# Optimization experiments

Measured on AMD Instinct MI355X. Metric: run time of the kernel, lower is better.

The kernel has to match this reference:

```python
import jax, jax.numpy as jnp
import numpy as np

N = 100_000      # nodes
E = 3_200_000    # directed edges (avg degree 32)
F_IN = 503
C = 32           # GATConv out_channels, heads=1
NEG_SLOPE = 0.2  # PyG GATConv default


def setup_inputs() -> dict:
    key = jax.random.key(0)
    ks = jax.random.split(key, 14)
    x = jax.random.normal(ks[0], (N, F_IN), jnp.float32)
    edge_index = jax.random.randint(ks[1], (2, E), 0, N)
    edge_weight = jax.random.uniform(ks[2], (E, 1), jnp.float32)
    input_mask = jnp.ones((N, 1), jnp.float32)
    # GATConv params (heads=1)
    W_src = jax.random.normal(ks[3], (C, F_IN), jnp.float32) * 0.02
    att_src = jax.random.normal(ks[4], (C,), jnp.float32) * 0.1
    att_dst = jax.random.normal(ks[5], (C,), jnp.float32) * 0.1
    att_edge = jax.random.normal(ks[6], (C,), jnp.float32) * 0.1
    W_edge = jax.random.normal(ks[7], (C, 1), jnp.float32) * 0.1
    bias_conv = jnp.zeros((C,), jnp.float32)
    # dense heads
    Wb = jax.random.normal(ks[8], (1, C), jnp.float32) * 0.1
    bb = jnp.zeros((1,), jnp.float32)
    Ww = jax.random.normal(ks[9], (1, C), jnp.float32) * 0.1
    bw = jnp.zeros((1,), jnp.float32)
    return {"x": x, "edge_index": edge_index, "edge_weight": edge_weight,
            "input_mask": input_mask, "W_src": W_src, "att_src": att_src,
            "att_dst": att_dst, "att_edge": att_edge, "W_edge": W_edge,
            "bias_conv": bias_conv, "Wb": Wb, "bb": bb, "Ww": Ww, "bw": bw}


def reference(x, edge_index, edge_weight, input_mask, W_src, att_src, att_dst,
              att_edge, W_edge, bias_conv, Wb, bb, Ww, bw):
    n = x.shape[0]
    xl = x @ W_src.T                       # [N, C] transformed node features
    a_src = xl @ att_src                   # [N] per-node source attention logit
    a_dst = xl @ att_dst                   # [N]
    src, dst = edge_index[0], edge_index[1]
    # add_self_loops=True with fill_value='mean' for edge_attr (PyG default)
    loop = jnp.arange(n)
    mean_attr = jnp.mean(edge_weight, axis=0, keepdims=True)      # [1,1]
    ea = jnp.concatenate([edge_weight, jnp.broadcast_to(mean_attr, (n, 1))], 0)
    s = jnp.concatenate([src, loop])       # [E+N]
    d = jnp.concatenate([dst, loop])
    a_edge = (ea @ W_edge.T) @ att_edge    # [E+N]
    alpha = jax.nn.leaky_relu(a_src[s] + a_dst[d] + a_edge, NEG_SLOPE)
    # softmax over incoming edges of each destination node
    amax = jax.ops.segment_max(alpha, d, num_segments=n)
    ex = jnp.exp(alpha - amax[d])
    denom = jax.ops.segment_sum(ex, d, num_segments=n)
    w = ex / denom[d]                      # [E+N] attention coeffs
    msg = xl[s] * w[:, None]               # [E+N, C]
    out = jax.ops.segment_sum(msg, d, num_segments=n) + bias_conv  # [N, C]
    h = jax.nn.relu(out)
    biases = (h @ Wb.T + bb) * input_mask  # [N, 1]
    weights = ((h[src] + h[dst]) * 0.5) @ Ww.T + bw  # [E, 1]
    return weights, biases
```

## Files before the change

kernel.cpp:

```cpp
#include <hip/hip_runtime.h>
#include <stdint.h>

#define NN 100000
#define NE 3200000
#define FIN 503
#define COUT 32
#define NSLOPE 0.2f

#define BSH 6
#define NB 1563
#define NGB 1563
#define NHB 400
#define EPB (NE / NHB)
#define NSB 7
#define MAXBE 2560

typedef __bf16 bf16x8 __attribute__((ext_vector_type(8)));
typedef float  f32x4  __attribute__((ext_vector_type(4)));

__device__ __forceinline__ unsigned short bf1(float f) {
    unsigned u = __float_as_uint(f);
    u = (u + 0x7FFFu + ((u >> 16) & 1u)) >> 16;
    return (unsigned short)u;
}
__device__ __forceinline__ float unbf(unsigned short h) {
    return __uint_as_float(((unsigned)h) << 16);
}

#define GR 64

__global__ __launch_bounds__(256)
void k_fused1(const float* __restrict__ x, const float* __restrict__ W,
              const float* __restrict__ att_s, const float* __restrict__ att_d,
              unsigned short* __restrict__ xlb,
              float* __restrict__ a_src, float* __restrict__ a_dst,
              const int* __restrict__ ei_dst, const float* __restrict__ ew,
              float* __restrict__ partial, unsigned* __restrict__ part,
              unsigned* __restrict__ done)
{
    __shared__ __align__(16) unsigned short xs[2][GR][40];
    __shared__ __align__(16) unsigned short ws[2][32][40];
    const int t = threadIdx.x;

    if (blockIdx.x >= NGB) {
        unsigned* h = (unsigned*)&xs[0][0][0];
        __shared__ float wsum[4];
        const int hb = blockIdx.x - NGB;
        for (int i = t; i < NB; i += 256) h[i] = 0u;
        __syncthreads();
        const int base = hb * EPB;
        for (int i = t; i < EPB; i += 256)
            atomicAdd(&h[ei_dst[base + i] >> BSH], 1u);
        const float4* ew4 = (const float4*)ew;
        float s = 0.f;
        for (int i = hb * 256 + t; i < NE / 4; i += NHB * 256) {
            float4 v = ew4[i];
            s += v.x + v.y + v.z + v.w;
        }
        #pragma unroll
        for (int off = 32; off > 0; off >>= 1) s += __shfl_xor(s, off);
        if ((t & 63) == 0) wsum[t >> 6] = s;
        __syncthreads();
        if (t == 0) partial[hb] = wsum[0] + wsum[1] + wsum[2] + wsum[3];
        for (int i = t; i < NB; i += 256)
            part[(size_t)hb * NB + i] = h[i];
        return;
    }

    if (blockIdx.x == 0 && t == 0) *done = 0u;
    unsigned short* os = &xs[0][0][0];
    const int wv = t >> 6, lane = t & 63;
    const int m16 = lane & 15, quad = lane >> 4;
    const int row0 = blockIdx.x * GR;
    const int srow = t >> 5;
    const int scol = t & 31;
    const int rowf = wv * 16 + m16;
    const int wrow = t >> 3;
    const int wc   = (t & 7) * 4;

    auto stageX = [&](int ch, int buf) {
        const int k = ch * 32 + scol;
        const bool ok = (k < FIN);
        #pragma unroll
        for (int p = 0; p < 8; ++p) {
            int r = p * 8 + srow;
            int rg = row0 + r;
            rg = (rg < NN) ? rg : (NN - 1);
            xs[buf][r][scol] = bf1(ok ? x[(size_t)rg * FIN + k] : 0.f);
        }
    };
    auto stageW = [&](int ch, int buf) {
        const int kb = ch * 32 + wc;
        #pragma unroll
        for (int j = 0; j < 4; ++j) {
            int k = kb + j;
            ws[buf][wrow][wc + j] = bf1((k < FIN) ? W[(size_t)wrow * FIN + k] : 0.f);
        }
    };

    f32x4 acc0 = {0.f, 0.f, 0.f, 0.f};
    f32x4 acc1 = {0.f, 0.f, 0.f, 0.f};

    stageX(0, 0);
    stageW(0, 0);
    for (int ch = 0; ch < 16; ++ch) {
        __syncthreads();
        if (ch < 15) {
            stageX(ch + 1, (ch + 1) & 1);
            stageW(ch + 1, (ch + 1) & 1);
        }
        bf16x8 af  = *(const bf16x8*)&xs[ch & 1][rowf][quad * 8];
        bf16x8 b0f = *(const bf16x8*)&ws[ch & 1][m16][quad * 8];
        bf16x8 b1f = *(const bf16x8*)&ws[ch & 1][m16 + 16][quad * 8];
        acc0 = __builtin_amdgcn_mfma_f32_16x16x32_bf16(af, b0f, acc0, 0, 0, 0);
        acc1 = __builtin_amdgcn_mfma_f32_16x16x32_bf16(af, b1f, acc1, 0, 0, 0);
    }

    #pragma unroll
    for (int r = 0; r < 4; ++r) {
        int rr = wv * 16 + quad * 4 + r;
        os[rr * 40 + m16]      = bf1(acc0[r]);
        os[rr * 40 + 16 + m16] = bf1(acc1[r]);
    }
    __syncthreads();
    {
        int r = t >> 2, c0 = (t & 3) * 8;
        int grow = row0 + r;
        uint4 o = *(const uint4*)&os[r * 40 + c0];
        float s = 0.f, dd = 0.f;
        const unsigned short* oh = (const unsigned short*)&o;
        #pragma unroll
        for (int j = 0; j < 8; ++j) {
            float v = unbf(oh[j]);
            s  += v * att_s[c0 + j];
            dd += v * att_d[c0 + j];
        }
        s  += __shfl_xor(s, 1, 4);  s  += __shfl_xor(s, 2, 4);
        dd += __shfl_xor(dd, 1, 4); dd += __shfl_xor(dd, 2, 4);
        if (grow < NN) {
            *(uint4*)&xlb[(size_t)grow * COUT + c0] = o;
            if ((t & 3) == 0) { a_src[grow] = s; a_dst[grow] = dd; }
        }
    }
}

__global__ __launch_bounds__(256)
void k_scan(unsigned* __restrict__ part, unsigned* __restrict__ colsum,
            unsigned* __restrict__ done, const float* __restrict__ partial,
            const float* __restrict__ W_edge, const float* __restrict__ att_e,
            float* __restrict__ stats, unsigned* __restrict__ bbase)
{
    const int t = threadIdx.x;
    const int bkt = blockIdx.x * 256 + t;
    if (bkt < NB) {
        unsigned run = 0u;
        #pragma unroll 1
        for (int s = 0; s < NHB; s += 8) {
            unsigned v[8];
            #pragma unroll
            for (int j = 0; j < 8; ++j) v[j] = part[(size_t)(s + j) * NB + bkt];
            #pragma unroll
            for (int j = 0; j < 8; ++j) {
                part[(size_t)(s + j) * NB + bkt] = run;
                run += v[j];
            }
        }
        colsum[bkt] = run;
    }
    __threadfence();
    __syncthreads();
    __shared__ unsigned winner;
    if (t == 0) winner = atomicAdd(done, 1u);
    __syncthreads();
    if (winner != NSB - 1) return;

    __shared__ float fs[256];
    fs[t] = (t < NHB ? partial[t] : 0.f) + (t + 256 < NHB ? partial[t + 256] : 0.f);
    __syncthreads();
    for (int off = 128; off > 0; off >>= 1) {
        if (t < off) fs[t] += fs[t + off];
        __syncthreads();
    }
    if (t == 0) {
        stats[0] = fs[0];
        float k = 0.f;
        for (int c = 0; c < COUT; ++c) k += W_edge[c] * att_e[c];
        stats[1] = k;
    }
    __syncthreads();
    __shared__ unsigned sm[256];
    __shared__ unsigned carry;
    if (t == 0) carry = 0u;
    __syncthreads();
    for (int c0 = 0; c0 < NB; c0 += 256) {
        int i = c0 + t;
        unsigned cv = (i < NB) ? atomicAdd(&colsum[i], 0u) : 0u;
        sm[t] = cv;
        for (int off = 1; off < 256; off <<= 1) {
            __syncthreads();
            unsigned tv = (t >= off) ? sm[t - off] : 0u;
            __syncthreads();
            sm[t] += tv;
        }
        __syncthreads();
        if (i < NB) bbase[i] = carry + sm[t] - cv;
        __syncthreads();
        if (t == 0) carry += sm[255];
        __syncthreads();
    }
    if (t == 0) bbase[NB] = carry;
}

__global__ __launch_bounds__(256)
void k_scatter(const int* __restrict__ ei, const float* __restrict__ ew,
               const float* __restrict__ a_src, const float* __restrict__ stats,
               const unsigned* __restrict__ part, const unsigned* __restrict__ bbase,
               uint2* __restrict__ csr)
{
    __shared__ unsigned cur[NB];
    const int b = blockIdx.x;
    const int t = threadIdx.x;
    for (int i = t; i < NB; i += 256)
        cur[i] = bbase[i] + part[(size_t)b * NB + i];
    __syncthreads();
    const float kc = stats[1];
    const int base = b * EPB;
    for (int i = t; i < EPB; i += 256) {
        int e = base + i;
        int s = ei[e];
        int d = ei[NE + e];
        float pre = a_src[s] + kc * ew[e];
        unsigned pos = atomicAdd(&cur[d >> BSH], 1u);
        csr[pos] = make_uint2((unsigned)s | ((unsigned)(d & 63) << 20),
                              __float_as_uint(pre));
    }
}

__global__ __launch_bounds__(256)
void k_aggr(const uint2* __restrict__ csr, const unsigned* __restrict__ bbase,
            const float* __restrict__ a_src, const float* __restrict__ a_dst,
            const unsigned short* __restrict__ xlb, const float* __restrict__ stats,
            const float* __restrict__ bias_conv, const float* __restrict__ Wb,
            const float* __restrict__ bb, const float* __restrict__ Ww,
            const float* __restrict__ mask, float* __restrict__ out_b,
            float* __restrict__ hw)
{
    __shared__ uint2 rec[MAXBE];
    __shared__ unsigned seg[65], cur[64];
    const int t = threadIdx.x;
    const int b = blockIdx.x;
    const int jb = (int)bbase[b];
    int ne = (int)bbase[b + 1] - jb;
    if (ne > MAXBE) ne = MAXBE;

    if (t < 64) cur[t] = 0u;
    __syncthreads();
    for (int i = t; i < ne; i += 256)
        atomicAdd(&cur[csr[jb + i].x >> 20], 1u);
    __syncthreads();
    if (t < 64) {
        unsigned v = cur[t];
        unsigned s = v;
        #pragma unroll
        for (int off = 1; off < 64; off <<= 1) {
            unsigned u = __shfl_up(s, off, 64);
            if (t >= off) s += u;
        }
        seg[t + 1] = s;
        cur[t] = s - v;
        if (t == 0) seg[0] = 0u;
    }
    __syncthreads();
    for (int i = t; i < ne; i += 256) {
        uint2 r = csr[jb + i];
        unsigned pos = atomicAdd(&cur[r.x >> 20], 1u);
        rec[pos] = r;
    }
    __syncthreads();

    const float kmean = stats[1] * (stats[0] * (1.f / NE));
    const int lane = t & 31;
    for (int dl = t >> 5; dl < 64; dl += 8) {
        int d = (b << BSH) + dl;
        if (d >= NN) continue;
        const float adv = a_dst[d];
        float a0 = a_src[d] + adv + kmean;
        a0 = (a0 > 0.f) ? a0 : NSLOPE * a0;
        const float ps = __expf(a0);
        float l = 0.f;
        float acc = ps * unbf(xlb[(size_t)d * COUT + lane]);
        const int j0 = (int)seg[dl], j1 = (int)seg[dl + 1];
        for (int tb = j0; tb < j1; tb += 32) {
            int j = tb + lane;
            float p = 0.f;
            if (j < j1) {
                uint2 en = rec[j];
                float a = __uint_as_float(en.y) + adv;
                a = (a > 0.f) ? a : NSLOPE * a;
                p = __expf(a);
                rec[j].y = __float_as_uint(p);
            }
            l += p;
            int cnte = min(32, j1 - tb);
            #pragma unroll 4
            for (int k = 0; k < cnte; ++k) {
                uint2 en = rec[tb + k];
                acc += __uint_as_float(en.y) *
                       unbf(xlb[(size_t)(en.x & 0xFFFFFu) * COUT + lane]);
            }
        }
        #pragma unroll
        for (int off = 16; off > 0; off >>= 1) l += __shfl_xor(l, off, 32);
        l += ps;
        float h = fmaxf(acc / l + bias_conv[lane], 0.f);
        float pb = h * Wb[lane];
        float pw = h * Ww[lane];
        #pragma unroll
        for (int off = 16; off > 0; off >>= 1) {
            pb += __shfl_xor(pb, off, 32);
            pw += __shfl_xor(pw, off, 32);
        }
        if (lane == 0) {
            out_b[d] = (pb + bb[0]) * mask[d];
            hw[d] = pw;
        }
    }
}

__global__ void k_weights(const int* __restrict__ ei, const float* __restrict__ hw,
                          const float* __restrict__ bw, float* __restrict__ out_w)
{
    int e4 = blockIdx.x * 256 + threadIdx.x;
    if (e4 < NE / 4) {
        int4 s4 = ((const int4*)ei)[e4];
        int4 d4 = ((const int4*)(ei + NE))[e4];
        float bwv = bw[0];
        float4 o;
        o.x = 0.5f * (hw[s4.x] + hw[d4.x]) + bwv;
        o.y = 0.5f * (hw[s4.y] + hw[d4.y]) + bwv;
        o.z = 0.5f * (hw[s4.z] + hw[d4.z]) + bwv;
        o.w = 0.5f * (hw[s4.w] + hw[d4.w]) + bwv;
        ((float4*)out_w)[e4] = o;
    }
}

extern "C" void kernel_launch(void* const* d_in, const int* in_sizes, int n_in,
                              void* d_out, int out_size, void* d_ws, size_t ws_size,
                              hipStream_t stream)
{
    const float* x        = (const float*)d_in[0];
    const int*   ei       = (const int*)d_in[1];
    const float* ew       = (const float*)d_in[2];
    const float* mask     = (const float*)d_in[3];
    const float* W_src    = (const float*)d_in[4];
    const float* att_src  = (const float*)d_in[5];
    const float* att_dst  = (const float*)d_in[6];
    const float* att_edge = (const float*)d_in[7];
    const float* W_edge   = (const float*)d_in[8];
    const float* bias_c   = (const float*)d_in[9];
    const float* Wb       = (const float*)d_in[10];
    const float* bb       = (const float*)d_in[11];
    const float* Ww       = (const float*)d_in[12];
    const float* bw       = (const float*)d_in[13];
    (void)in_sizes; (void)n_in; (void)out_size; (void)ws_size;

    char* wsp = (char*)d_ws;
    size_t off = 0;
    auto alloc = [&](size_t bytes) -> void* {
        void* p = wsp + off;
        off = (off + bytes + 255) & ~(size_t)255;
        return p;
    };
    unsigned short* xlb    = (unsigned short*)alloc((size_t)NN * COUT * 2);
    float*    a_src  = (float*)alloc((size_t)NN * 4);
    float*    a_dst  = (float*)alloc((size_t)NN * 4);
    float*    stats  = (float*)alloc(256);
    float*    partial= (float*)alloc((size_t)NHB * 4);
    unsigned* part   = (unsigned*)alloc((size_t)NHB * NB * 4);
    unsigned* colsum = (unsigned*)alloc((size_t)NB * 4);
    unsigned* bbase  = (unsigned*)alloc((size_t)(NB + 1) * 4);
    unsigned* done   = (unsigned*)alloc(256);
    uint2*    csr    = (uint2*)alloc((size_t)NE * 8);
    float*    hw     = (float*)alloc((size_t)NN * 4);

    float* out_w = (float*)d_out;
    float* out_b = out_w + NE;

    k_fused1  <<<NGB + NHB, 256, 0, stream>>>(x, W_src, att_src, att_dst,
                                              xlb, a_src, a_dst,
                                              ei + NE, ew, partial, part, done);
    k_scan    <<<NSB, 256, 0, stream>>>(part, colsum, done, partial, W_edge,
                                        att_edge, stats, bbase);
    k_scatter <<<NHB, 256, 0, stream>>>(ei, ew, a_src, stats, part, bbase, csr);
    k_aggr    <<<NB, 256, 0, stream>>>(csr, bbase, a_src, a_dst, xlb, stats,
                                       bias_c, Wb, bb, Ww, mask, out_b, hw);
    k_weights <<<NE / 4 / 256, 256, 0, stream>>>(ei, hw, bw, out_w);
}
```

Before: 546.2 us.

## Prefetch GEMM chunks into registers, widen histogram grid, split edge loop across half-waves

The GEMM staging now loads the next K-chunk into registers before the MFMAs and writes it to LDS afterwards, leaving one barrier per iteration, so global-load latency overlaps with compute. The histogram phase uses 1000 blocks instead of 400, and the final partial reduction loops over all partials. The aggregation kernel assigns one 64-lane wave per destination node, with each 32-lane half processing alternate edge batches and the halves combined by a cross-half shuffle. Costs are more registers in the GEMM and fewer destination nodes processed concurrently per block.

Result: slower. 611.3 us (+11.9%).

```diff
diff --git a/kernel.cpp b/kernel.cpp
--- a/kernel.cpp
+++ b/kernel.cpp
@@ -10,7 +10,7 @@
 #define BSH 6
 #define NB 1563
 #define NGB 1563
-#define NHB 400
+#define NHB 1000
 #define EPB (NE / NHB)
 #define NSB 7
 #define MAXBE 2560
@@ -78,42 +78,46 @@
     const int wrow = t >> 3;
     const int wc   = (t & 7) * 4;
 
-    auto stageX = [&](int ch, int buf) {
+    float xv[8];
+    float wvr[4];
+    auto loadChunk = [&](int ch) {
         const int k = ch * 32 + scol;
         const bool ok = (k < FIN);
         #pragma unroll
         for (int p = 0; p < 8; ++p) {
-            int r = p * 8 + srow;
-            int rg = row0 + r;
+            int rg = row0 + p * 8 + srow;
             rg = (rg < NN) ? rg : (NN - 1);
-            xs[buf][r][scol] = bf1(ok ? x[(size_t)rg * FIN + k] : 0.f);
+            xv[p] = ok ? x[(size_t)rg * FIN + k] : 0.f;
+        }
+        const int kb = ch * 32 + wc;
+        #pragma unroll
+        for (int j = 0; j < 4; ++j) {
+            int kk = kb + j;
+            wvr[j] = (kk < FIN) ? W[(size_t)wrow * FIN + kk] : 0.f;
         }
     };
-    auto stageW = [&](int ch, int buf) {
-        const int kb = ch * 32 + wc;
-        #pragma unroll
-        for (int j = 0; j < 4; ++j) {
-            int k = kb + j;
-            ws[buf][wrow][wc + j] = bf1((k < FIN) ? W[(size_t)wrow * FIN + k] : 0.f);
-        }
+    auto writeStage = [&](int buf) {
+        #pragma unroll
+        for (int p = 0; p < 8; ++p) xs[buf][p * 8 + srow][scol] = bf1(xv[p]);
+        #pragma unroll
+        for (int j = 0; j < 4; ++j) ws[buf][wrow][wc + j] = bf1(wvr[j]);
     };
 
     f32x4 acc0 = {0.f, 0.f, 0.f, 0.f};
     f32x4 acc1 = {0.f, 0.f, 0.f, 0.f};
 
-    stageX(0, 0);
-    stageW(0, 0);
+    loadChunk(0);
+    writeStage(0);
+    __syncthreads();
     for (int ch = 0; ch < 16; ++ch) {
-        __syncthreads();
-        if (ch < 15) {
-            stageX(ch + 1, (ch + 1) & 1);
-            stageW(ch + 1, (ch + 1) & 1);
-        }
+        if (ch < 15) loadChunk(ch + 1);
         bf16x8 af  = *(const bf16x8*)&xs[ch & 1][rowf][quad * 8];
         bf16x8 b0f = *(const bf16x8*)&ws[ch & 1][m16][quad * 8];
         bf16x8 b1f = *(const bf16x8*)&ws[ch & 1][m16 + 16][quad * 8];
         acc0 = __builtin_amdgcn_mfma_f32_16x16x32_bf16(af, b0f, acc0, 0, 0, 0);
         acc1 = __builtin_amdgcn_mfma_f32_16x16x32_bf16(af, b1f, acc1, 0, 0, 0);
+        if (ch < 15) writeStage((ch + 1) & 1);
+        __syncthreads();
     }
 
     #pragma unroll
@@ -175,7 +179,11 @@
     if (winner != NSB - 1) return;
 
     __shared__ float fs[256];
-    fs[t] = (t < NHB ? partial[t] : 0.f) + (t + 256 < NHB ? partial[t + 256] : 0.f);
+    {
+        float ps = 0.f;
+        for (int i = t; i < NHB; i += 256) ps += partial[i];
+        fs[t] = ps;
+    }
     __syncthreads();
     for (int off = 128; off > 0; off >>= 1) {
         if (t < off) fs[t] += fs[t + off];
@@ -279,8 +287,10 @@
     __syncthreads();
 
     const float kmean = stats[1] * (stats[0] * (1.f / NE));
-    const int lane = t & 31;
-    for (int dl = t >> 5; dl < 64; dl += 8) {
+    const int lane32 = t & 31;
+    const int half = (t >> 5) & 1;
+    const int wid = t >> 6;
+    for (int dl = wid; dl < 64; dl += 4) {
         int d = (b << BSH) + dl;
         if (d >= NN) continue;
         const float adv = a_dst[d];
@@ -288,10 +298,10 @@
         a0 = (a0 > 0.f) ? a0 : NSLOPE * a0;
         const float ps = __expf(a0);
         float l = 0.f;
-        float acc = ps * unbf(xlb[(size_t)d * COUT + lane]);
+        float acc = (half == 0) ? ps * unbf(xlb[(size_t)d * COUT + lane32]) : 0.f;
         const int j0 = (int)seg[dl], j1 = (int)seg[dl + 1];
-        for (int tb = j0; tb < j1; tb += 32) {
-            int j = tb + lane;
+        for (int tb = j0 + half * 32; tb < j1; tb += 64) {
+            int j = tb + lane32;
             float p = 0.f;
             if (j < j1) {
                 uint2 en = rec[j];
@@ -306,21 +316,23 @@
             for (int k = 0; k < cnte; ++k) {
                 uint2 en = rec[tb + k];
                 acc += __uint_as_float(en.y) *
-                       unbf(xlb[(size_t)(en.x & 0xFFFFFu) * COUT + lane]);
+                       unbf(xlb[(size_t)(en.x & 0xFFFFFu) * COUT + lane32]);
             }
         }
         #pragma unroll
         for (int off = 16; off > 0; off >>= 1) l += __shfl_xor(l, off, 32);
+        l += __shfl_xor(l, 32, 64);
+        acc += __shfl_xor(acc, 32, 64);
         l += ps;
-        float h = fmaxf(acc / l + bias_conv[lane], 0.f);
-        float pb = h * Wb[lane];
-        float pw = h * Ww[lane];
+        float h = fmaxf(acc / l + bias_conv[lane32], 0.f);
+        float pb = h * Wb[lane32];
+        float pw = h * Ww[lane32];
         #pragma unroll
         for (int off = 16; off > 0; off >>= 1) {
             pb += __shfl_xor(pb, off, 32);
             pw += __shfl_xor(pw, off, 32);
         }
-        if (lane == 0) {
+        if ((t & 63) == 0) {
             out_b[d] = (pb + bb[0]) * mask[d];
             hw[d] = pw;
         }
```
